# Optimization experiments

Measured on AMD Instinct MI355X. Metric: run time of the kernel, lower is better.

Reference implementation:

```python
import jax, jax.numpy as jnp
import numpy as np

DIM = 192
TDIM = 192
HEADS = 6
WS = (2, 7, 7)
SS = (1, 3, 3)
MLP_HID = 4 * DIM
RANK = DIM // 8
EPS = 1e-6


def _rel_pos_index(ws):
    wd, wh, ww = ws
    coords = np.stack(np.meshgrid(np.arange(wd), np.arange(wh), np.arange(ww), indexing='ij'))
    cf = coords.reshape(3, -1)
    rel = (cf[:, :, None] - cf[:, None, :]).transpose(1, 2, 0).astype(np.int64)
    rel[..., 0] += wd - 1
    rel[..., 1] += wh - 1
    rel[..., 2] += ww - 1
    rel[..., 0] *= (2 * wh - 1) * (2 * ww - 1)
    rel[..., 1] *= (2 * ww - 1)
    return rel.sum(-1)  # (N, N)


def _window_partition(x, ws):
    B, D, H, W, C = x.shape
    x = x.reshape(B, D // ws[0], ws[0], H // ws[1], ws[1], W // ws[2], ws[2], C)
    return x.transpose(0, 1, 3, 5, 2, 4, 6, 7).reshape(-1, ws[0] * ws[1] * ws[2], C)


def _window_reverse(w, ws, B, D, H, W):
    x = w.reshape(B, D // ws[0], H // ws[1], W // ws[2], ws[0], ws[1], ws[2], -1)
    return x.transpose(0, 1, 4, 2, 5, 3, 6, 7).reshape(B, D, H, W, -1)


def _ln(x):
    m = x.mean(-1, keepdims=True)
    v = ((x - m) ** 2).mean(-1, keepdims=True)
    return (x - m) * jax.lax.rsqrt(v + EPS)


def _compute_mask_np(Dp, Hp, Wp, ws, ss):
    img = np.zeros((1, Dp, Hp, Wp, 1), dtype=np.float32)
    cnt = 0
    for d in (slice(0, -ws[0]), slice(-ws[0], -ss[0]), slice(-ss[0], None)):
        for h in (slice(0, -ws[1]), slice(-ws[1], -ss[1]), slice(-ss[1], None)):
            for w in (slice(0, -ws[2]), slice(-ws[2], -ss[2]), slice(-ss[2], None)):
                img[:, d, h, w, :] = cnt
                cnt += 1
    x = img.reshape(1, Dp // ws[0], ws[0], Hp // ws[1], ws[1], Wp // ws[2], ws[2], 1)
    mw = x.transpose(0, 1, 3, 5, 2, 4, 6, 7).reshape(-1, ws[0] * ws[1] * ws[2])
    am = mw[:, None, :] - mw[:, :, None]
    return np.where(am != 0, np.float32(-100.0), np.float32(0.0))


def setup_inputs() -> dict:
    key = jax.random.key(0)
    ks = jax.random.split(key, 16)
    B, D, H, W, C = 1, 16, 64, 128, DIM
    Dp = D + (-D) % WS[0]
    Hp = H + (-H) % WS[1]
    Wp = W + (-W) % WS[2]
    s = 0.02
    bias_tab = (2 * WS[0] - 1) * (2 * WS[1] - 1) * (2 * WS[2] - 1)
    return {
        'x': jax.random.normal(ks[0], (B, D, H, W, C), jnp.float32),
        'mask_matrix': jnp.asarray(_compute_mask_np(Dp, Hp, Wp, WS, SS)),
        't': jax.random.normal(ks[1], (B, TDIM), jnp.float32),
        'w_qkv': jax.random.normal(ks[2], (C, 3 * C), jnp.float32) * s,
        'b_qkv': jnp.zeros((3 * C,), jnp.float32),
        'rel_bias': jax.random.normal(ks[3], (bias_tab, HEADS), jnp.float32) * s,
        'w_proj': jax.random.normal(ks[4], (C, C), jnp.float32) * s,
        'b_proj': jnp.zeros((C,), jnp.float32),
        'w1': jax.random.normal(ks[5], (C, MLP_HID), jnp.float32) * s,
        'b1': jnp.zeros((MLP_HID,), jnp.float32),
        'w2': jax.random.normal(ks[6], (MLP_HID, C), jnp.float32) * s,
        'b2': jnp.zeros((C,), jnp.float32),
        'wa1': jax.random.normal(ks[7], (TDIM, RANK), jnp.float32) * s,
        'wa2': jax.random.normal(ks[8], (RANK, 6 * C), jnp.float32) * s,
        'ba2': jax.random.normal(ks[9], (6 * C,), jnp.float32) * s,
    }


def reference(x, mask_matrix, t, w_qkv, b_qkv, rel_bias, w_proj, b_proj, w1, b1, w2, b2, wa1, wa2, ba2):
    B, D, H, W, C = x.shape
    hd = C // HEADS
    # AdaLN modulation params
    mod = (jax.nn.silu(t) @ wa1) @ wa2 + ba2  # (B, 6C)
    sh_msa, sc_msa, g_msa, sh_mlp, sc_mlp, g_mlp = jnp.split(mod, 6, axis=1)

    def modulate(y, sh, sc):
        return y * (1 + sc[:, None, None, None, :]) + sh[:, None, None, None, :]

    shortcut = x
    y = modulate(_ln(x), sh_msa, sc_msa)
    # pad to window multiples
    pad_d, pad_h, pad_w = (-D) % WS[0], (-H) % WS[1], (-W) % WS[2]
    y = jnp.pad(y, ((0, 0), (0, pad_d), (0, pad_h), (0, pad_w), (0, 0)))
    Dp, Hp, Wp = D + pad_d, H + pad_h, W + pad_w
    # cyclic shift
    y = jnp.roll(y, (-SS[0], -SS[1], -SS[2]), axis=(1, 2, 3))
    xw = _window_partition(y, WS)  # (B*nW, N, C)
    N = xw.shape[1]
    qkv = (xw @ w_qkv + b_qkv).reshape(-1, N, 3, HEADS, hd)
    q, k, v = qkv[:, :, 0], qkv[:, :, 1], qkv[:, :, 2]
    scale = hd ** -0.5
    attn = jnp.einsum('bnhd,bmhd->bhnm', q * scale, k)  # (B*nW, H, N, N)
    rpi = _rel_pos_index(WS)
    bias = rel_bias[rpi.reshape(-1)].reshape(N, N, HEADS).transpose(2, 0, 1)
    attn = attn + bias[None]
    nW = mask_matrix.shape[0]
    attn = attn.reshape(B, nW, HEADS, N, N) + mask_matrix[None, :, None]
    attn = jax.nn.softmax(attn, axis=-1).reshape(-1, HEADS, N, N)
    out = jnp.einsum('bhnm,bmhd->bnhd', attn, v).reshape(-1, N, C)
    out = out @ w_proj + b_proj
    y = _window_reverse(out, WS, B, Dp, Hp, Wp)
    y = jnp.roll(y, (SS[0], SS[1], SS[2]), axis=(1, 2, 3))
    y = y[:, :D, :H, :W, :]
    x1 = shortcut + g_msa[:, None, None, None, :] * y
    y2 = modulate(_ln(x1), sh_mlp, sc_mlp)
    h = jax.nn.gelu(y2 @ w1 + b1, approximate=False) @ w2 + b2
    return x1 + g_mlp[:, None, None, None, :] * h
```

## Files before the change

### kernel.cpp

```cpp
#include <hip/hip_runtime.h>
#include <hip/hip_bf16.h>

typedef __bf16 bf16x8 __attribute__((ext_vector_type(8)));
typedef float  f32x4  __attribute__((ext_vector_type(4)));
typedef unsigned int u32x4 __attribute__((ext_vector_type(4)));

__device__ inline unsigned short f2bf(float f) {
    union { __hip_bfloat16 h; unsigned short u; } cv;
    cv.h = __float2bfloat16(f);
    return cv.u;
}
__device__ inline float bf2f(unsigned short u) {
    union { unsigned int i; float f; } c; c.i = ((unsigned int)u) << 16; return c.f;
}

__device__ inline bf16x8 load8(const unsigned short* p) {
    uint2 lo = *(const uint2*)(p);
    uint2 hi = *(const uint2*)(p + 16);
    u32x4 v; v[0] = lo.x; v[1] = lo.y; v[2] = hi.x; v[3] = hi.y;
    return __builtin_bit_cast(bf16x8, v);
}

__device__ inline f32x4 mfma16(bf16x8 a, bf16x8 b, f32x4 c) {
    return __builtin_amdgcn_mfma_f32_16x16x32_bf16(a, b, c, 0, 0, 0);
}

__device__ inline bool winmapT(int gg, int& T) {
    int win = gg / 98, n = gg % 98;
    int wdi = win / 190, rem = win % 190, whi = rem / 19, wwi = rem % 19;
    int td = n / 49, th = (n / 7) % 7, tw = n % 7;
    int sd = (wdi * 2 + td + 1) & 15;
    int sh = whi * 7 + th + 3; if (sh >= 70) sh -= 70;
    int sw = wwi * 7 + tw + 3; if (sw >= 133) sw -= 133;
    if (sh < 64 && sw < 128) { T = (sd * 64 + sh) * 128 + sw; return true; }
    return false;
}

__global__ __launch_bounds__(256) void mod_k(const float* __restrict__ t,
    const float* __restrict__ wa1, const float* __restrict__ wa2,
    const float* __restrict__ ba2, float* __restrict__ mod)
{
    __shared__ float st[192];
    __shared__ float a[24];
    int tid = threadIdx.x;
    if (tid < 192) { float x = t[tid]; st[tid] = x / (1.f + __expf(-x)); }
    __syncthreads();
    if (tid < 24) {
        float s = 0.f;
        for (int c = 0; c < 192; ++c) s += st[c] * wa1[c * 24 + tid];
        a[tid] = s;
    }
    __syncthreads();
    for (int j = tid; j < 1152; j += 256) {
        float s = ba2[j];
        for (int r = 0; r < 24; ++r) s += a[r] * wa2[r * 1152 + j];
        mod[j] = s;
    }
}

__global__ __launch_bounds__(256) void prep_k(
    const float* __restrict__ wqkv, const float* __restrict__ wproj,
    const float* __restrict__ w1, const float* __restrict__ w2,
    const float* __restrict__ relb,
    unsigned short* __restrict__ wqkvT, unsigned short* __restrict__ wprojT,
    unsigned short* __restrict__ w1T, unsigned short* __restrict__ w2T,
    unsigned short* __restrict__ btabF)
{
    int i = blockIdx.x * 256 + threadIdx.x;
    if (i < 110592) { int n = i / 192, k = i % 192; wqkvT[i] = f2bf(wqkv[k * 576 + n]); return; }
    i -= 110592;
    if (i < 36864)  { int n = i / 192, k = i % 192; wprojT[i] = f2bf(wproj[k * 192 + n]); return; }
    i -= 36864;
    if (i < 147456) { int n = i / 192, k = i % 192; w1T[i] = f2bf(w1[k * 768 + n]); return; }
    i -= 147456;
    if (i < 147456) { int n = i / 768, k = i % 768; w2T[i] = f2bf(w2[k * 192 + n]); return; }
    i -= 147456;
    if (i < 688128) {
        int mt = i / 86016, r1 = i % 86016;
        int h  = r1 / 14336, r2 = r1 % 14336;
        int fq = r2 / 2048,  r3 = r2 % 2048;
        int l16 = r3 / 128,  r4 = r3 % 128;
        int lg  = r4 / 32,   r5 = r4 % 32;
        int fkey = r5 / 4,   e  = r5 % 4;
        int q = fq * 16 + l16, key = fkey * 16 + lg * 4 + e;
        float val;
        if (fkey == 7 || q >= 98 || key >= 98) {
            val = -1e30f;
        } else {
            int tdn = q / 49, thn = (q / 7) % 7, twn = q % 7;
            int tdm = key / 49, thm = (key / 7) % 7, twm = key % 7;
            int idx = (tdn - tdm + 1) * 169 + (thn - thm + 6) * 13 + (twn - twm + 6);
            float b = relb[idx * 6 + h];
            int bd = mt & 1, bh = (mt >> 1) & 1, bw = (mt >> 2) & 1;
            int idn = (bd ? (tdn == 0 ? 1 : 2) : 0) * 9 + (bh ? (thn < 4 ? 1 : 2) : 0) * 3 + (bw ? (twn < 4 ? 1 : 2) : 0);
            int idm = (bd ? (tdm == 0 ? 1 : 2) : 0) * 9 + (bh ? (thm < 4 ? 1 : 2) : 0) * 3 + (bw ? (twm < 4 ? 1 : 2) : 0);
            val = b + ((idn != idm) ? -100.f : 0.f);
        }
        btabF[i] = f2bf(val);
    }
}

__global__ __launch_bounds__(256) void stats_f32_k(const float* __restrict__ x,
    float* __restrict__ st)
{
    int tok = blockIdx.x * 4 + (threadIdx.x >> 6);
    int lane = threadIdx.x & 63;
    const float* p = x + (size_t)tok * 192;
    float a = p[lane], b = p[64 + lane], c = p[128 + lane];
    float s = a + b + c, q = a * a + b * b + c * c;
    for (int m = 32; m; m >>= 1) { s += __shfl_xor(s, m); q += __shfl_xor(q, m); }
    if (lane == 0) {
        float mean = s * (1.f / 192.f);
        float var  = q * (1.f / 192.f) - mean * mean;
        st[2 * tok] = mean;
        st[2 * tok + 1] = rsqrtf(var + 1e-6f);
    }
}

template<int FN, int STAGE, int EPI>
__global__ __launch_bounds__(256) void gemm_k(
    const unsigned short* __restrict__ A, const float* __restrict__ Af,
    const unsigned short* __restrict__ BT, const float* __restrict__ bias,
    unsigned short* __restrict__ outB, float* outF,
    const float* __restrict__ auxF, const float* __restrict__ stats,
    const float* __restrict__ mod, int row0, int M, int N, int K)
{
    constexpr int BN = FN * 32;
    __shared__ unsigned short As[128][44];
    __shared__ unsigned short Bs[BN][44];
    const int t = threadIdx.x;
    const int n0 = blockIdx.x * BN, m0 = blockIdx.y * 128;
    const int lr = t >> 2, lk = (t & 3) * 8;
    const int wid = t >> 6, lane = t & 63;
    const int lg = lane >> 4, l16 = lane & 15;
    const int wm = (wid >> 1) * 64, wn = (wid & 1) * (FN * 16);
    f32x4 acc[4][FN] = {};

    float mn[2] = {0.f, 0.f}, rs[2] = {0.f, 0.f};
    size_t sbase[2] = {0, 0};
    bool va[2] = {false, false};
    #pragma unroll
    for (int rr = 0; rr < 2; ++rr) {
        int g = m0 + lr + rr * 64;
        if (STAGE == 1) {
            int T;
            if (g < M && winmapT(row0 + g, T)) {
                va[rr] = true; sbase[rr] = (size_t)T * 192;
                mn[rr] = stats[2 * T]; rs[rr] = stats[2 * T + 1];
            }
        } else if (STAGE == 2) {
            int tok = row0 + g;
            sbase[rr] = (size_t)tok * 192;
            mn[rr] = stats[2 * tok]; rs[rr] = stats[2 * tok + 1];
        }
    }

    for (int kk = 0; kk < K; kk += 32) {
        #pragma unroll
        for (int rr = 0; rr < 2; ++rr) {
            int r = lr + rr * 64;
            int g = m0 + r;
            uint4 w = make_uint4(0u, 0u, 0u, 0u);
            if (STAGE == 0) {
                if (g < M) w = *(const uint4*)(A + (size_t)g * K + kk + lk);
            } else if (STAGE == 1) {
                if (va[rr]) {
                    float4 xa = *(const float4*)(Af + sbase[rr] + kk + lk);
                    float4 xb = *(const float4*)(Af + sbase[rr] + kk + lk + 4);
                    float xs[8] = {xa.x, xa.y, xa.z, xa.w, xb.x, xb.y, xb.z, xb.w};
                    unsigned short o[8];
                    #pragma unroll
                    for (int j = 0; j < 8; ++j) {
                        int c = kk + lk + j;
                        o[j] = f2bf((xs[j] - mn[rr]) * rs[rr] * (1.f + mod[192 + c]) + mod[c]);
                    }
                    w = make_uint4((unsigned)o[0] | ((unsigned)o[1] << 16), (unsigned)o[2] | ((unsigned)o[3] << 16),
                                   (unsigned)o[4] | ((unsigned)o[5] << 16), (unsigned)o[6] | ((unsigned)o[7] << 16));
                }
            } else {
                float4 xa = *(const float4*)(Af + sbase[rr] + kk + lk);
                float4 xb = *(const float4*)(Af + sbase[rr] + kk + lk + 4);
                float xs[8] = {xa.x, xa.y, xa.z, xa.w, xb.x, xb.y, xb.z, xb.w};
                unsigned short o[8];
                #pragma unroll
                for (int j = 0; j < 8; ++j) {
                    int c = kk + lk + j;
                    o[j] = f2bf((xs[j] - mn[rr]) * rs[rr] * (1.f + mod[768 + c]) + mod[576 + c]);
                }
                w = make_uint4((unsigned)o[0] | ((unsigned)o[1] << 16), (unsigned)o[2] | ((unsigned)o[3] << 16),
                               (unsigned)o[4] | ((unsigned)o[5] << 16), (unsigned)o[6] | ((unsigned)o[7] << 16));
            }
            *(uint2*)(&As[r][lk])     = make_uint2(w.x, w.y);
            *(uint2*)(&As[r][lk + 4]) = make_uint2(w.z, w.w);
        }
        #pragma unroll
        for (int rr = 0; rr < BN / 64; ++rr) {
            int r = lr + rr * 64;
            int gn = n0 + r;
            uint4 w = make_uint4(0u, 0u, 0u, 0u);
            if (gn < N) w = *(const uint4*)(BT + (size_t)gn * K + kk + lk);
            *(uint2*)(&Bs[r][lk])     = make_uint2(w.x, w.y);
            *(uint2*)(&Bs[r][lk + 4]) = make_uint2(w.z, w.w);
        }
        __syncthreads();
        bf16x8 af[4], bv[FN];
        #pragma unroll
        for (int i = 0; i < 4; ++i) af[i] = load8(&As[wm + i * 16 + l16][4 * lg]);
        #pragma unroll
        for (int j = 0; j < FN; ++j) bv[j] = load8(&Bs[wn + j * 16 + l16][4 * lg]);
        #pragma unroll
        for (int i = 0; i < 4; ++i)
        #pragma unroll
        for (int j = 0; j < FN; ++j)
            acc[i][j] = mfma16(af[i], bv[j], acc[i][j]);
        __syncthreads();
    }

    #pragma unroll
    for (int i = 0; i < 4; ++i)
    #pragma unroll
    for (int j = 0; j < FN; ++j) {
        int gcol = n0 + wn + j * 16 + l16;
        if (gcol >= N) continue;
        float b = bias[gcol];
        #pragma unroll
        for (int e = 0; e < 4; ++e) {
            int grow = m0 + wm + i * 16 + lg * 4 + e;
            if (grow >= M) continue;
            float v = acc[i][j][e] + b;
            if (EPI == 0) {
                int which = gcol / 192, hh = (gcol / 32) % 6, c = gcol & 31;
                outB[((size_t)(hh * 3 + which) * 148960 + grow) * 32 + c] = f2bf(v);
            } else if (EPI == 1) {
                float gl = 0.5f * v * (1.f + erff(v * 0.70710678118654752f));
                outB[(size_t)grow * N + gcol] = f2bf(gl);
            } else if (EPI == 2) {
                int T;
                if (winmapT(row0 + grow, T)) {
                    size_t idx = (size_t)T * 192 + gcol;
                    outF[idx] = auxF[idx] + mod[384 + gcol] * v;
                }
            } else {
                size_t idx = (size_t)(row0 + grow) * 192 + gcol;
                outF[idx] = outF[idx] + mod[960 + gcol] * v;
            }
        }
    }
}

__global__ __launch_bounds__(256) void attn_k(
    const unsigned short* __restrict__ qkv, const unsigned short* __restrict__ btabF,
    unsigned short* __restrict__ out)
{
    __shared__ __align__(16) unsigned short Ks[112 * 46];
    __shared__ __align__(16) unsigned short VT[32 * 142];

    const int blk = blockIdx.x;
    const int win = blk / 6, h = blk % 6;
    const int t = threadIdx.x;
    const int wid = t >> 6, lg = (t >> 4) & 3, l16 = t & 15;
    const size_t rb = (size_t)win * 98;

    const unsigned short* Qg = qkv + (size_t)(h * 3 + 0) * 148960 * 32;
    const unsigned short* Kg = qkv + (size_t)(h * 3 + 1) * 148960 * 32;
    const unsigned short* Vg = qkv + (size_t)(h * 3 + 2) * 148960 * 32;

    const int wdi = win / 190, remw = win % 190, whi = remw / 19, wwi = remw % 19;
    const int mt = (wdi == 7 ? 1 : 0) | (whi == 9 ? 2 : 0) | (wwi == 18 ? 4 : 0);
    const unsigned short* btF = btabF + (size_t)(mt * 6 + h) * 14336;

    for (int i = t; i < 392; i += 256) {
        int r = i >> 2, cg = (i & 3) * 8;
        uint4 k = *(const uint4*)(Kg + (rb + r) * 32 + cg);
        *(uint2*)(Ks + r * 46 + cg)     = make_uint2(k.x, k.y);
        *(uint2*)(Ks + r * 46 + cg + 4) = make_uint2(k.z, k.w);
    }
    for (int i = t; i < 14 * 32; i += 256) {
        int r = 98 + (i >> 5), c = i & 31;
        Ks[r * 46 + c] = 0;
    }
    if (t < 392) {
        uint4 v = *(const uint4*)(Vg + (rb + (t >> 2)) * 32 + (t & 3) * 8);
        const unsigned short* vp = (const unsigned short*)&v;
        int m = t >> 2, c0 = (t & 3) * 8;
        #pragma unroll
        for (int j = 0; j < 8; ++j) VT[(c0 + j) * 142 + m] = vp[j];
    }
    {
        int t2 = t + 256;
        if (t2 < 392) {
            uint4 v = *(const uint4*)(Vg + (rb + (t2 >> 2)) * 32 + (t2 & 3) * 8);
            const unsigned short* vp = (const unsigned short*)&v;
            int m = t2 >> 2, c0 = (t2 & 3) * 8;
            #pragma unroll
            for (int j = 0; j < 8; ++j) VT[(c0 + j) * 142 + m] = vp[j];
        }
    }
    for (int i = t; i < 32 * 30; i += 256) { int c = i / 30, m = 98 + i % 30; VT[c * 142 + m] = 0; }
    __syncthreads();

    __builtin_amdgcn_s_setprio(1);
    const float SCALE = 0.17677669529663687f;
    #pragma unroll
    for (int fi = 0; fi < 2; ++fi) {
        const int fq = wid + fi * 4;
        if (fq >= 7) break;

        const uint4* bp = (const uint4*)(btF + fq * 2048 + l16 * 128 + lg * 32);
        uint4 b0 = bp[0], b1 = bp[1], b2 = bp[2], b3 = bp[3];
        const unsigned bt32[16] = {b0.x, b0.y, b0.z, b0.w, b1.x, b1.y, b1.z, b1.w,
                                   b2.x, b2.y, b2.z, b2.w, b3.x, b3.y, b3.z, b3.w};

        bf16x8 qa = load8(Qg + (rb + fq * 16 + l16) * 32 + 4 * lg);
        f32x4 acc[7];
        #pragma unroll
        for (int fk = 0; fk < 7; ++fk) {
            bf16x8 kb = load8(Ks + (fk * 16 + l16) * 46 + 4 * lg);
            f32x4 z = {};
            acc[fk] = mfma16(kb, qa, z);
        }

        float mx = -1e30f;
        #pragma unroll
        for (int fk = 0; fk < 7; ++fk)
        #pragma unroll
        for (int e = 0; e < 4; ++e) {
            unsigned short bu = (unsigned short)(bt32[fk * 2 + (e >> 1)] >> ((e & 1) * 16));
            float s = fmaf(acc[fk][e], SCALE, bf2f(bu));
            acc[fk][e] = s;
            mx = fmaxf(mx, s);
        }
        mx = fmaxf(mx, __shfl_xor(mx, 16));
        mx = fmaxf(mx, __shfl_xor(mx, 32));
        float sum = 0.f;
        #pragma unroll
        for (int fk = 0; fk < 7; ++fk)
        #pragma unroll
        for (int e = 0; e < 4; ++e) {
            float p = __expf(acc[fk][e] - mx);
            acc[fk][e] = p;
            sum += p;
        }
        sum += __shfl_xor(sum, 16);
        sum += __shfl_xor(sum, 32);
        float rinv = 1.f / sum;

        bf16x8 sa[4];
        #pragma unroll
        for (int ks = 0; ks < 4; ++ks) {
            u32x4 w;
            w[0] = (unsigned)f2bf(acc[2 * ks][0]) | ((unsigned)f2bf(acc[2 * ks][1]) << 16);
            w[1] = (unsigned)f2bf(acc[2 * ks][2]) | ((unsigned)f2bf(acc[2 * ks][3]) << 16);
            if (ks < 3) {
                w[2] = (unsigned)f2bf(acc[2 * ks + 1][0]) | ((unsigned)f2bf(acc[2 * ks + 1][1]) << 16);
                w[3] = (unsigned)f2bf(acc[2 * ks + 1][2]) | ((unsigned)f2bf(acc[2 * ks + 1][3]) << 16);
            } else {
                w[2] = 0u; w[3] = 0u;
            }
            sa[ks] = __builtin_bit_cast(bf16x8, w);
        }
        float rv[4];
        #pragma unroll
        for (int e = 0; e < 4; ++e) rv[e] = __shfl(rinv, lg * 4 + e);

        #pragma unroll
        for (int fn = 0; fn < 2; ++fn) {
            f32x4 o = {};
            #pragma unroll
            for (int ks = 0; ks < 4; ++ks) {
                bf16x8 vb = load8(VT + (fn * 16 + l16) * 142 + ks * 32 + 4 * lg);
                o = mfma16(sa[ks], vb, o);
            }
            #pragma unroll
            for (int e = 0; e < 4; ++e) {
                int r = fq * 16 + lg * 4 + e;
                if (r < 98) {
                    out[(rb + r) * 192 + h * 32 + fn * 16 + l16] = f2bf(o[e] * rv[e]);
                }
            }
        }
    }
    __builtin_amdgcn_s_setprio(0);
}

extern "C" void kernel_launch(void* const* d_in, const int* in_sizes, int n_in,
                              void* d_out, int out_size, void* d_ws, size_t ws_size,
                              hipStream_t stream)
{
    const float* x      = (const float*)d_in[0];
    const float* tvec   = (const float*)d_in[2];
    const float* w_qkv  = (const float*)d_in[3];
    const float* b_qkv  = (const float*)d_in[4];
    const float* relb   = (const float*)d_in[5];
    const float* w_proj = (const float*)d_in[6];
    const float* b_proj = (const float*)d_in[7];
    const float* w1     = (const float*)d_in[8];
    const float* b1     = (const float*)d_in[9];
    const float* w2     = (const float*)d_in[10];
    const float* b2     = (const float*)d_in[11];
    const float* wa1    = (const float*)d_in[12];
    const float* wa2    = (const float*)d_in[13];
    const float* ba2    = (const float*)d_in[14];

    char* ws = (char*)d_ws;
    float*          mod    = (float*)ws;
    float*          stats1 = (float*)(ws + 4608);
    float*          stats2 = (float*)(ws + 1053184);
    unsigned short* wqkvT  = (unsigned short*)(ws + 2101760);
    unsigned short* wprojT = (unsigned short*)(ws + 2322944);
    unsigned short* w1T    = (unsigned short*)(ws + 2396672);
    unsigned short* w2T    = (unsigned short*)(ws + 2691584);
    unsigned short* btabF  = (unsigned short*)(ws + 2986496);
    unsigned short* qkvb   = (unsigned short*)(ws + 4834304);
    unsigned short* h      = (unsigned short*)(ws + 4834304);
    unsigned short* attn_c = (unsigned short*)(ws + 176436224);
    float*          dout   = (float*)d_out;

    mod_k<<<1, 256, 0, stream>>>(tvec, wa1, wa2, ba2, mod);
    prep_k<<<4416, 256, 0, stream>>>(w_qkv, w_proj, w1, w2, relb, wqkvT, wprojT, w1T, w2T, btabF);
    stats_f32_k<<<32768, 256, 0, stream>>>(x, stats1);

    gemm_k<4, 1, 0><<<dim3(5, 1164), 256, 0, stream>>>(
        nullptr, x, wqkvT, b_qkv, qkvb, nullptr, nullptr, stats1, mod, 0, 148960, 576, 192);
    attn_k<<<9120, 256, 0, stream>>>(qkvb, btabF, attn_c);
    gemm_k<2, 0, 2><<<dim3(3, 1164), 256, 0, stream>>>(
        attn_c, nullptr, wprojT, b_proj, nullptr, dout, x, nullptr, mod, 0, 148960, 192, 192);

    stats_f32_k<<<32768, 256, 0, stream>>>(dout, stats2);

    gemm_k<4, 2, 1><<<dim3(6, 1024), 256, 0, stream>>>(
        nullptr, dout, w1T, b1, h, nullptr, nullptr, stats2, mod, 0, 131072, 768, 192);
    gemm_k<2, 0, 3><<<dim3(3, 1024), 256, 0, stream>>>(
        h, nullptr, w2T, b2, nullptr, dout, nullptr, nullptr, mod, 0, 131072, 192, 768);
}
```

Baseline: 1.010 ms.

## Precompute LayerNorm+modulate into bf16 buffers, add XCD swizzle, prefetch attention operands

```diff
diff --git a/kernel.cpp b/kernel.cpp
--- a/kernel.cpp
+++ b/kernel.cpp
@@ -34,6 +34,12 @@
     int sw = wwi * 7 + tw + 3; if (sw >= 133) sw -= 133;
     if (sh < 64 && sw < 128) { T = (sd * 64 + sh) * 128 + sw; return true; }
     return false;
+}
+
+__device__ inline int xcd_swz(int orig, int nwg) {
+    int q = nwg >> 3, r = nwg & 7;
+    int xcd = orig & 7, idx = orig >> 3;
+    return (xcd < r ? xcd * (q + 1) : r * (q + 1) + (xcd - r) * q) + idx;
 }
 
 __global__ __launch_bounds__(256) void mod_k(const float* __restrict__ t,
@@ -100,98 +106,74 @@
     }
 }
 
-__global__ __launch_bounds__(256) void stats_f32_k(const float* __restrict__ x,
-    float* __restrict__ st)
+__global__ __launch_bounds__(256) void lnwin_k(const float* __restrict__ x,
+    const float* __restrict__ mod, unsigned short* __restrict__ ywin)
 {
     int tok = blockIdx.x * 4 + (threadIdx.x >> 6);
     int lane = threadIdx.x & 63;
-    const float* p = x + (size_t)tok * 192;
-    float a = p[lane], b = p[64 + lane], c = p[128 + lane];
-    float s = a + b + c, q = a * a + b * b + c * c;
-    for (int m = 32; m; m >>= 1) { s += __shfl_xor(s, m); q += __shfl_xor(q, m); }
-    if (lane == 0) {
+    int T;
+    size_t ob = (size_t)tok * 192;
+    if (winmapT(tok, T)) {
+        const float* p = x + (size_t)T * 192;
+        float x0 = p[lane], xa = p[64 + lane], xb = p[128 + lane];
+        float s = x0 + xa + xb, q = x0 * x0 + xa * xa + xb * xb;
+        for (int m = 32; m; m >>= 1) { s += __shfl_xor(s, m); q += __shfl_xor(q, m); }
         float mean = s * (1.f / 192.f);
         float var  = q * (1.f / 192.f) - mean * mean;
-        st[2 * tok] = mean;
-        st[2 * tok + 1] = rsqrtf(var + 1e-6f);
-    }
-}
-
-template<int FN, int STAGE, int EPI>
+        float rstd = rsqrtf(var + 1e-6f);
+        ywin[ob + lane]       = f2bf((x0 - mean) * rstd * (1.f + mod[192 + lane])       + mod[lane]);
+        ywin[ob + 64 + lane]  = f2bf((xa - mean) * rstd * (1.f + mod[192 + 64 + lane])  + mod[64 + lane]);
+        ywin[ob + 128 + lane] = f2bf((xb - mean) * rstd * (1.f + mod[192 + 128 + lane]) + mod[128 + lane]);
+    } else {
+        ywin[ob + lane] = 0; ywin[ob + 64 + lane] = 0; ywin[ob + 128 + lane] = 0;
+    }
+}
+
+__global__ __launch_bounds__(256) void ln2_k(const float* __restrict__ x1,
+    const float* __restrict__ mod, unsigned short* __restrict__ y2)
+{
+    int tok = blockIdx.x * 4 + (threadIdx.x >> 6);
+    int lane = threadIdx.x & 63;
+    const float* p = x1 + (size_t)tok * 192;
+    float x0 = p[lane], xa = p[64 + lane], xb = p[128 + lane];
+    float s = x0 + xa + xb, q = x0 * x0 + xa * xa + xb * xb;
+    for (int m = 32; m; m >>= 1) { s += __shfl_xor(s, m); q += __shfl_xor(q, m); }
+    float mean = s * (1.f / 192.f);
+    float var  = q * (1.f / 192.f) - mean * mean;
+    float rstd = rsqrtf(var + 1e-6f);
+    size_t ob = (size_t)tok * 192;
+    y2[ob + lane]       = f2bf((x0 - mean) * rstd * (1.f + mod[768 + lane])       + mod[576 + lane]);
+    y2[ob + 64 + lane]  = f2bf((xa - mean) * rstd * (1.f + mod[768 + 64 + lane])  + mod[576 + 64 + lane]);
+    y2[ob + 128 + lane] = f2bf((xb - mean) * rstd * (1.f + mod[768 + 128 + lane]) + mod[576 + 128 + lane]);
+}
+
+template<int FN, int EPI>
 __global__ __launch_bounds__(256) void gemm_k(
-    const unsigned short* __restrict__ A, const float* __restrict__ Af,
-    const unsigned short* __restrict__ BT, const float* __restrict__ bias,
-    unsigned short* __restrict__ outB, float* outF,
-    const float* __restrict__ auxF, const float* __restrict__ stats,
-    const float* __restrict__ mod, int row0, int M, int N, int K)
+    const unsigned short* __restrict__ A, const unsigned short* __restrict__ BT,
+    const float* __restrict__ bias, unsigned short* __restrict__ outB, float* outF,
+    const float* __restrict__ auxF, const float* __restrict__ mod,
+    int M, int N, int K, int nx)
 {
     constexpr int BN = FN * 32;
-    __shared__ unsigned short As[128][44];
-    __shared__ unsigned short Bs[BN][44];
+    __shared__ unsigned short As[128][40];
+    __shared__ unsigned short Bs[BN][40];
     const int t = threadIdx.x;
-    const int n0 = blockIdx.x * BN, m0 = blockIdx.y * 128;
+    const int wg = xcd_swz(blockIdx.x, gridDim.x);
+    const int n0 = (wg % nx) * BN, m0 = (wg / nx) * 128;
     const int lr = t >> 2, lk = (t & 3) * 8;
     const int wid = t >> 6, lane = t & 63;
     const int lg = lane >> 4, l16 = lane & 15;
     const int wm = (wid >> 1) * 64, wn = (wid & 1) * (FN * 16);
     f32x4 acc[4][FN] = {};
 
-    float mn[2] = {0.f, 0.f}, rs[2] = {0.f, 0.f};
-    size_t sbase[2] = {0, 0};
-    bool va[2] = {false, false};
-    #pragma unroll
-    for (int rr = 0; rr < 2; ++rr) {
-        int g = m0 + lr + rr * 64;
-        if (STAGE == 1) {
-            int T;
-            if (g < M && winmapT(row0 + g, T)) {
-                va[rr] = true; sbase[rr] = (size_t)T * 192;
-                mn[rr] = stats[2 * T]; rs[rr] = stats[2 * T + 1];
-            }
-        } else if (STAGE == 2) {
-            int tok = row0 + g;
-            sbase[rr] = (size_t)tok * 192;
-            mn[rr] = stats[2 * tok]; rs[rr] = stats[2 * tok + 1];
-        }
-    }
-
     for (int kk = 0; kk < K; kk += 32) {
         #pragma unroll
         for (int rr = 0; rr < 2; ++rr) {
             int r = lr + rr * 64;
             int g = m0 + r;
             uint4 w = make_uint4(0u, 0u, 0u, 0u);
-            if (STAGE == 0) {
-                if (g < M) w = *(const uint4*)(A + (size_t)g * K + kk + lk);
-            } else if (STAGE == 1) {
-                if (va[rr]) {
-                    float4 xa = *(const float4*)(Af + sbase[rr] + kk + lk);
-                    float4 xb = *(const float4*)(Af + sbase[rr] + kk + lk + 4);
-                    float xs[8] = {xa.x, xa.y, xa.z, xa.w, xb.x, xb.y, xb.z, xb.w};
-                    unsigned short o[8];
-                    #pragma unroll
-                    for (int j = 0; j < 8; ++j) {
-                        int c = kk + lk + j;
-                        o[j] = f2bf((xs[j] - mn[rr]) * rs[rr] * (1.f + mod[192 + c]) + mod[c]);
-                    }
-                    w = make_uint4((unsigned)o[0] | ((unsigned)o[1] << 16), (unsigned)o[2] | ((unsigned)o[3] << 16),
-                                   (unsigned)o[4] | ((unsigned)o[5] << 16), (unsigned)o[6] | ((unsigned)o[7] << 16));
-                }
-            } else {
-                float4 xa = *(const float4*)(Af + sbase[rr] + kk + lk);
-                float4 xb = *(const float4*)(Af + sbase[rr] + kk + lk + 4);
-                float xs[8] = {xa.x, xa.y, xa.z, xa.w, xb.x, xb.y, xb.z, xb.w};
-                unsigned short o[8];
-                #pragma unroll
-                for (int j = 0; j < 8; ++j) {
-                    int c = kk + lk + j;
-                    o[j] = f2bf((xs[j] - mn[rr]) * rs[rr] * (1.f + mod[768 + c]) + mod[576 + c]);
-                }
-                w = make_uint4((unsigned)o[0] | ((unsigned)o[1] << 16), (unsigned)o[2] | ((unsigned)o[3] << 16),
-                               (unsigned)o[4] | ((unsigned)o[5] << 16), (unsigned)o[6] | ((unsigned)o[7] << 16));
-            }
-            *(uint2*)(&As[r][lk])     = make_uint2(w.x, w.y);
-            *(uint2*)(&As[r][lk + 4]) = make_uint2(w.z, w.w);
+            if (g < M) w = *(const uint4*)(A + (size_t)g * K + kk + lk);
+            *(uint4*)(&As[r][lk]) = w;
         }
         #pragma unroll
         for (int rr = 0; rr < BN / 64; ++rr) {
@@ -199,8 +181,7 @@
             int gn = n0 + r;
             uint4 w = make_uint4(0u, 0u, 0u, 0u);
             if (gn < N) w = *(const uint4*)(BT + (size_t)gn * K + kk + lk);
-            *(uint2*)(&Bs[r][lk])     = make_uint2(w.x, w.y);
-            *(uint2*)(&Bs[r][lk + 4]) = make_uint2(w.z, w.w);
+            *(uint4*)(&Bs[r][lk]) = w;
         }
         __syncthreads();
         bf16x8 af[4], bv[FN];
@@ -236,12 +217,12 @@
                 outB[(size_t)grow * N + gcol] = f2bf(gl);
             } else if (EPI == 2) {
                 int T;
-                if (winmapT(row0 + grow, T)) {
+                if (winmapT(grow, T)) {
                     size_t idx = (size_t)T * 192 + gcol;
                     outF[idx] = auxF[idx] + mod[384 + gcol] * v;
                 }
             } else {
-                size_t idx = (size_t)(row0 + grow) * 192 + gcol;
+                size_t idx = (size_t)grow * 192 + gcol;
                 outF[idx] = outF[idx] + mod[960 + gcol] * v;
             }
         }
@@ -255,8 +236,8 @@
     __shared__ __align__(16) unsigned short Ks[112 * 46];
     __shared__ __align__(16) unsigned short VT[32 * 142];
 
-    const int blk = blockIdx.x;
-    const int win = blk / 6, h = blk % 6;
+    const int wg = xcd_swz(blockIdx.x, 9120);
+    const int h = wg / 1520, win = wg % 1520;
     const int t = threadIdx.x;
     const int wid = t >> 6, lg = (t >> 4) & 3, l16 = t & 15;
     const size_t rb = (size_t)win * 98;
@@ -268,6 +249,17 @@
     const int wdi = win / 190, remw = win % 190, whi = remw / 19, wwi = remw % 19;
     const int mt = (wdi == 7 ? 1 : 0) | (whi == 9 ? 2 : 0) | (wwi == 18 ? 4 : 0);
     const unsigned short* btF = btabF + (size_t)(mt * 6 + h) * 14336;
+
+    bf16x8 qa[2];
+    uint4 btr[2][4];
+    #pragma unroll
+    for (int fi = 0; fi < 2; ++fi) {
+        int fq = wid + fi * 4;
+        int fqc = (fq < 7) ? fq : 0;
+        qa[fi] = load8(Qg + (rb + fqc * 16 + l16) * 32 + 4 * lg);
+        const uint4* bp = (const uint4*)(btF + fqc * 2048 + l16 * 128 + lg * 32);
+        btr[fi][0] = bp[0]; btr[fi][1] = bp[1]; btr[fi][2] = bp[2]; btr[fi][3] = bp[3];
+    }
 
     for (int i = t; i < 392; i += 256) {
         int r = i >> 2, cg = (i & 3) * 8;
@@ -306,18 +298,17 @@
         const int fq = wid + fi * 4;
         if (fq >= 7) break;
 
-        const uint4* bp = (const uint4*)(btF + fq * 2048 + l16 * 128 + lg * 32);
-        uint4 b0 = bp[0], b1 = bp[1], b2 = bp[2], b3 = bp[3];
-        const unsigned bt32[16] = {b0.x, b0.y, b0.z, b0.w, b1.x, b1.y, b1.z, b1.w,
-                                   b2.x, b2.y, b2.z, b2.w, b3.x, b3.y, b3.z, b3.w};
-
-        bf16x8 qa = load8(Qg + (rb + fq * 16 + l16) * 32 + 4 * lg);
+        const unsigned bt32[16] = {btr[fi][0].x, btr[fi][0].y, btr[fi][0].z, btr[fi][0].w,
+                                   btr[fi][1].x, btr[fi][1].y, btr[fi][1].z, btr[fi][1].w,
+                                   btr[fi][2].x, btr[fi][2].y, btr[fi][2].z, btr[fi][2].w,
+                                   btr[fi][3].x, btr[fi][3].y, btr[fi][3].z, btr[fi][3].w};
+
         f32x4 acc[7];
         #pragma unroll
         for (int fk = 0; fk < 7; ++fk) {
             bf16x8 kb = load8(Ks + (fk * 16 + l16) * 46 + 4 * lg);
             f32x4 z = {};
-            acc[fk] = mfma16(kb, qa, z);
+            acc[fk] = mfma16(kb, qa[fi], z);
         }
 
         float mx = -1e30f;
@@ -404,8 +395,6 @@
 
     char* ws = (char*)d_ws;
     float*          mod    = (float*)ws;
-    float*          stats1 = (float*)(ws + 4608);
-    float*          stats2 = (float*)(ws + 1053184);
     unsigned short* wqkvT  = (unsigned short*)(ws + 2101760);
     unsigned short* wprojT = (unsigned short*)(ws + 2322944);
     unsigned short* w1T    = (unsigned short*)(ws + 2396672);
@@ -414,22 +403,24 @@
     unsigned short* qkvb   = (unsigned short*)(ws + 4834304);
     unsigned short* h      = (unsigned short*)(ws + 4834304);
     unsigned short* attn_c = (unsigned short*)(ws + 176436224);
+    unsigned short* ywin   = (unsigned short*)(ws + 233636864);
+    unsigned short* y2b    = (unsigned short*)(ws + 290837504);
     float*          dout   = (float*)d_out;
 
     mod_k<<<1, 256, 0, stream>>>(tvec, wa1, wa2, ba2, mod);
     prep_k<<<4416, 256, 0, stream>>>(w_qkv, w_proj, w1, w2, relb, wqkvT, wprojT, w1T, w2T, btabF);
-    stats_f32_k<<<32768, 256, 0, stream>>>(x, stats1);
-
-    gemm_k<4, 1, 0><<<dim3(5, 1164), 256, 0, stream>>>(
-        nullptr, x, wqkvT, b_qkv, qkvb, nullptr, nullptr, stats1, mod, 0, 148960, 576, 192);
+    lnwin_k<<<37240, 256, 0, stream>>>(x, mod, ywin);
+
+    gemm_k<4, 0><<<5 * 1164, 256, 0, stream>>>(
+        ywin, wqkvT, b_qkv, qkvb, nullptr, nullptr, mod, 148960, 576, 192, 5);
     attn_k<<<9120, 256, 0, stream>>>(qkvb, btabF, attn_c);
-    gemm_k<2, 0, 2><<<dim3(3, 1164), 256, 0, stream>>>(
-        attn_c, nullptr, wprojT, b_proj, nullptr, dout, x, nullptr, mod, 0, 148960, 192, 192);
-
-    stats_f32_k<<<32768, 256, 0, stream>>>(dout, stats2);
-
-    gemm_k<4, 2, 1><<<dim3(6, 1024), 256, 0, stream>>>(
-        nullptr, dout, w1T, b1, h, nullptr, nullptr, stats2, mod, 0, 131072, 768, 192);
-    gemm_k<2, 0, 3><<<dim3(3, 1024), 256, 0, stream>>>(
-        h, nullptr, w2T, b2, nullptr, dout, nullptr, nullptr, mod, 0, 131072, 192, 768);
-}
+    gemm_k<2, 2><<<3 * 1164, 256, 0, stream>>>(
+        attn_c, wprojT, b_proj, nullptr, dout, x, mod, 148960, 192, 192, 3);
+
+    ln2_k<<<32768, 256, 0, stream>>>(dout, mod, y2b);
+
+    gemm_k<4, 1><<<6 * 1024, 256, 0, stream>>>(
+        y2b, w1T, b1, h, nullptr, nullptr, mod, 131072, 768, 192, 6);
+    gemm_k<2, 3><<<3 * 1024, 256, 0, stream>>>(
+        h, w2T, b2, nullptr, dout, nullptr, mod, 131072, 192, 768, 3);
+}
```

Measured after the change: 950.6 us. -5.9%, faster.
